# Performance work log

Hardware: AMD Instinct MI355X
Metric: run time of the kernel (lower is better)

The kernel has to match this reference:

```python
import jax, jax.numpy as jnp
import numpy as np

B_, S_, H_, O_ = 4, 2048, 2048, 2048
E_, R_ = 8, 16
LORA_ALPHA = 16.0


def setup_inputs() -> dict:
    key = jax.random.key(0)
    ks = jax.random.split(key, 5)
    x = jax.random.normal(ks[0], (B_, S_, H_), dtype=jnp.float32)
    W = jax.random.normal(ks[1], (O_, H_), dtype=jnp.float32) * 0.02   # frozen base weight [out, in]
    gate_w = jax.random.normal(ks[2], (E_, H_), dtype=jnp.float32) * 0.02  # router Linear weight [E, H]
    A = jax.random.normal(ks[3], (E_, R_, H_), dtype=jnp.float32) * 0.02   # stacked lora_A weights [E, r, in]
    B = jax.random.normal(ks[4], (E_, O_, R_), dtype=jnp.float32) * 0.02   # stacked lora_B weights [E, out, r]
    return {"x": x, "W": W, "gate_w": gate_w, "A": A, "B": B}


def reference(x, W, gate_w, A, B):
    bsz, seq, hid = x.shape
    E = gate_w.shape[0]
    x_flat = x.reshape(-1, hid)                                  # [T, H]

    # base linear
    out = x_flat @ W.T                                           # [T, O]

    # learned router: softmax -> top-2 -> renormalize
    logits = x_flat @ gate_w.T                                   # [T, E]
    probs = jax.nn.softmax(logits, axis=-1)
    topk_w, topk_idx = jax.lax.top_k(probs, 2)                   # [T, 2]
    topk_w = topk_w / jnp.sum(topk_w, axis=-1, keepdims=True)

    # per-token per-expert combine weight (sum over the 2 slots), scaled by alpha
    onehot = jax.nn.one_hot(topk_idx, E, dtype=x.dtype)          # [T, 2, E]
    wmat = jnp.einsum('tk,tke->te', topk_w, onehot) * LORA_ALPHA # [T, E]

    # dense grouped LoRA: h_e = x A_e^T ; out += sum_e w_te * (h_e B_e^T)
    h = jnp.einsum('th,erh->etr', x_flat, A)                     # [E, T, r]
    hw = h * wmat.T[:, :, None]                                  # [E, T, r]
    lora = jnp.einsum('etr,eor->to', hw, B)                      # [T, O]

    return (out + lora).reshape(bsz, seq, -1)
```

## Files before the change

### kernel.cpp

```cpp
#include <hip/hip_runtime.h>
#include <hip/hip_bf16.h>
#include <stdint.h>

#define T_TOK 8192
#define HID   2048
#define OUTD  2048
#define NE    8
#define RR    16
#define KAUG  2176
#define NH    128

typedef __bf16 bf16x8 __attribute__((ext_vector_type(8)));
typedef float  f32x4  __attribute__((ext_vector_type(4)));

#define AS1(p) ((__attribute__((address_space(1))) void*)(p))
#define AS3(p) ((__attribute__((address_space(3))) void*)(p))

__device__ inline unsigned short f2bf(float f) {
  unsigned int u = __builtin_bit_cast(unsigned int, f);
  unsigned int r = (u + 0x7fffu + ((u >> 16) & 1u)) >> 16;
  return (unsigned short)r;
}

__device__ inline ushort4 f2bf4(float4 v) {
  ushort4 u;
  u.x = f2bf(v.x); u.y = f2bf(v.y); u.z = f2bf(v.z); u.w = f2bf(v.w);
  return u;
}

__global__ __launch_bounds__(512) void k_prep(const float* __restrict__ x,
                                              const float* __restrict__ gw,
                                              const float* __restrict__ A,
                                              unsigned short* __restrict__ Xa,
                                              float* __restrict__ wte,
                                              unsigned short* __restrict__ Ag) {
  __shared__ float gws[NE * HID];
  if (blockIdx.x < 1024) {
#pragma unroll
    for (int i = 0; i < 8; ++i) {
      int idx = (i * 512 + (int)threadIdx.x) * 4;
      *(float4*)(gws + idx) = *(const float4*)(gw + idx);
    }
    __syncthreads();
    int w = threadIdx.x >> 6, lane = threadIdx.x & 63;
    int t = blockIdx.x * 8 + w;
    const float* xt = x + (size_t)t * HID;
    unsigned short* xo = Xa + (size_t)t * KAUG;
    double acc[8] = {0, 0, 0, 0, 0, 0, 0, 0};
#pragma unroll
    for (int i = 0; i < 8; ++i) {
      int k = (i * 64 + lane) * 4;
      float4 xv = *(const float4*)(xt + k);
      *(ushort4*)(xo + k) = f2bf4(xv);
#pragma unroll
      for (int e = 0; e < 8; ++e) {
        float4 gv = *(const float4*)(gws + e * HID + k);
        acc[e] += (double)xv.x * gv.x + (double)xv.y * gv.y +
                  (double)xv.z * gv.z + (double)xv.w * gv.w;
      }
    }
#pragma unroll
    for (int off = 32; off >= 1; off >>= 1)
#pragma unroll
      for (int e = 0; e < 8; ++e)
        acc[e] += __shfl_down(acc[e], off, 64);
    if (lane == 0) {
      int e0 = 0; double l0 = acc[0];
#pragma unroll
      for (int e = 1; e < 8; ++e) if (acc[e] > l0) { l0 = acc[e]; e0 = e; }
      int e1 = -1; double l1 = -1e300;
#pragma unroll
      for (int e = 0; e < 8; ++e) if (e != e0 && acc[e] > l1) { l1 = acc[e]; e1 = e; }
      double w0 = 16.0 / (1.0 + exp(l1 - l0));
      float o[8] = {0.f, 0.f, 0.f, 0.f, 0.f, 0.f, 0.f, 0.f};
      o[e0] = (float)w0;
      o[e1] = (float)(16.0 - w0);
      float4* p = (float4*)(wte + (size_t)t * 8);
      p[0] = make_float4(o[0], o[1], o[2], o[3]);
      p[1] = make_float4(o[4], o[5], o[6], o[7]);
    }
  } else {
    int tid = (blockIdx.x - 1024) * 512 + threadIdx.x;
    float4 v = *(const float4*)(A + (size_t)tid * 4);
    *(ushort4*)(Ag + (size_t)tid * 4) = f2bf4(v);
  }
}

__global__ __launch_bounds__(512) void k_ha(const unsigned short* __restrict__ Xa,
                                            const unsigned short* __restrict__ Ag,
                                            const float* __restrict__ wte,
                                            unsigned short* __restrict__ XaW,
                                            const float* __restrict__ W,
                                            const float* __restrict__ Bw,
                                            unsigned short* __restrict__ Wa) {
  __shared__ unsigned short Xs[4][32 * 64];
  __shared__ unsigned short As[4][128 * 64];
  if (blockIdx.x >= 256) {
    int b2 = blockIdx.x - 256;
    if (b2 < 2048) {
      int tid = b2 * 512 + threadIdx.x;
      int row = tid >> 9, c = (tid & 511) << 2;
      float4 v = *(const float4*)(W + (size_t)row * HID + c);
      *(ushort4*)(Wa + (size_t)row * KAUG + c) = f2bf4(v);
    } else {
      int tid = (b2 - 2048) * 512 + threadIdx.x;
      int o = tid >> 5, j = (tid & 31) << 2;
      int e = j >> 4, r = j & 15;
      float4 v = *(const float4*)(Bw + (size_t)e * OUTD * RR + (size_t)o * RR + r);
      *(ushort4*)(Wa + (size_t)o * KAUG + 2048 + j) = f2bf4(v);
    }
    return;
  }

  int tm = blockIdx.x * 32;
  int w = threadIdx.x >> 6, lane = threadIdx.x & 63;
  int wm = (w >> 2) * 16, wn = (w & 3) * 32;
  int lrow = lane >> 3;
  int lcol_s = (lane & 7) << 3;
  int lcol_g = ((lane & 7) ^ (lrow & 7)) << 3;

  const unsigned short* gX = Xa + (size_t)(tm + (w & 3) * 8 + lrow) * KAUG + lcol_g;
  const unsigned short* gA = Ag + (size_t)(w * 16 + lrow) * HID + lcol_g;
  int sxo = ((w & 3) * 8 + lrow) * 64 + lcol_s;
  int sao = (w * 16 + lrow) * 64 + lcol_s;

  f32x4 acc[2] = {};

#define HA_STAGE(slot, koff) do {                                                           \
    if (w < 4)                                                                              \
      __builtin_amdgcn_global_load_lds(AS1(gX + (koff)), AS3(&Xs[slot][0] + sxo), 16, 0, 0);\
    __builtin_amdgcn_global_load_lds(AS1(gA + (koff)), AS3(&As[slot][0] + sao), 16, 0, 0);  \
    __builtin_amdgcn_global_load_lds(AS1(gA + (size_t)8 * HID + (koff)),                    \
                                     AS3(&As[slot][0] + 8 * 64 + sao), 16, 0, 0);           \
  } while (0)

#define HA_COMP(s) do {                                                                     \
    _Pragma("unroll")                                                                       \
    for (int ks = 0; ks < 2; ++ks) {                                                        \
      int kch = ks * 4 + (lane >> 4);                                                       \
      int ko = ((kch ^ (lane & 7)) << 3);                         \
      bf16x8 a = *(const bf16x8*)(&Xs[s][0] + (wm + (lane & 15)) * 64 + ko);                \
      _Pragma("unroll")                                                                     \
      for (int fn = 0; fn < 2; ++fn) {                                                      \
        bf16x8 bv = *(const bf16x8*)(&As[s][0] + (wn + fn * 16 + (lane & 15)) * 64 + ko);   \
        acc[fn] = __builtin_amdgcn_mfma_f32_16x16x32_bf16(a, bv, acc[fn], 0, 0, 0);         \
      }                                                                                     \
    }                                                                                       \
  } while (0)

  HA_STAGE(0, 0);
  HA_STAGE(1, 64);
  HA_STAGE(2, 128);
  for (int t = 0; t < 29; ++t) {
    if (w < 4) asm volatile("s_waitcnt vmcnt(6)" ::: "memory");
    else       asm volatile("s_waitcnt vmcnt(4)" ::: "memory");
    __builtin_amdgcn_s_barrier();
    HA_COMP(t & 3);
    __builtin_amdgcn_s_barrier();
    HA_STAGE((t + 3) & 3, (t + 3) * 64);
  }
  if (w < 4) asm volatile("s_waitcnt vmcnt(6)" ::: "memory");
  else       asm volatile("s_waitcnt vmcnt(4)" ::: "memory");
  __builtin_amdgcn_s_barrier();
  HA_COMP(1);
  if (w < 4) asm volatile("s_waitcnt vmcnt(3)" ::: "memory");
  else       asm volatile("s_waitcnt vmcnt(2)" ::: "memory");
  __builtin_amdgcn_s_barrier();
  HA_COMP(2);
  asm volatile("s_waitcnt vmcnt(0)" ::: "memory");
  __builtin_amdgcn_s_barrier();
  HA_COMP(3);
#undef HA_STAGE
#undef HA_COMP

  int q = lane >> 4;
#pragma unroll
  for (int fn = 0; fn < 2; ++fn) {
    int col = wn + fn * 16 + (lane & 15);
    int e = col >> 4;
#pragma unroll
    for (int r = 0; r < 4; ++r) {
      int t = tm + wm + q * 4 + r;
      float we = wte[(size_t)t * 8 + e];
      XaW[(size_t)t * KAUG + 2048 + col] = f2bf(we * acc[fn][r]);
    }
  }
}

__global__ __launch_bounds__(256, 4) void k_gemm(const unsigned short* __restrict__ Xa,
                                                 const unsigned short* __restrict__ Wa,
                                                 float* __restrict__ out) {
  __shared__ unsigned short As[128 * 64];
  __shared__ unsigned short Bs[128 * 64];
  int lid = blockIdx.x;
  int xcd = lid & 7, s = lid >> 3;
  int bm = (xcd * 8 + (s & 7)) * 128;
  int bn = (s >> 3) * 128;
  int w = threadIdx.x >> 6, lane = threadIdx.x & 63;
  int wm = (w >> 1) * 64, wn = (w & 1) * 64;
  int lrow = lane >> 3;
  int lcol_s = (lane & 7) << 3;
  int lcol_g = ((lane & 7) ^ (lrow & 7)) << 3;

  const unsigned short* gA = Xa + (size_t)(bm + w * 32 + lrow) * KAUG + lcol_g;
  const unsigned short* gB = Wa + (size_t)(bn + w * 32 + lrow) * KAUG + lcol_g;
  unsigned short* sA = As + (w * 32 + lrow) * 64 + lcol_s;
  unsigned short* sB = Bs + (w * 32 + lrow) * 64 + lcol_s;

  f32x4 acc[4][4] = {};
  for (int kt = 0; kt < KAUG; kt += 64) {
#pragma unroll
    for (int i = 0; i < 4; ++i) {
      __builtin_amdgcn_global_load_lds(AS1(gA + (size_t)i * 8 * KAUG), AS3(sA + i * 8 * 64), 16, 0, 0);
      __builtin_amdgcn_global_load_lds(AS1(gB + (size_t)i * 8 * KAUG), AS3(sB + i * 8 * 64), 16, 0, 0);
    }
    __syncthreads();
#pragma unroll
    for (int ks = 0; ks < 2; ++ks) {
      int kch = ks * 4 + (lane >> 4);
      int ko = ((kch ^ (lane & 7)) << 3);
      bf16x8 a[4], b[4];
#pragma unroll
      for (int f = 0; f < 4; ++f) a[f] = *(const bf16x8*)(As + (wm + f * 16 + (lane & 15)) * 64 + ko);
#pragma unroll
      for (int f = 0; f < 4; ++f) b[f] = *(const bf16x8*)(Bs + (wn + f * 16 + (lane & 15)) * 64 + ko);
#pragma unroll
      for (int fm = 0; fm < 4; ++fm)
#pragma unroll
        for (int fn = 0; fn < 4; ++fn)
          acc[fm][fn] = __builtin_amdgcn_mfma_f32_16x16x32_bf16(a[fm], b[fn], acc[fm][fn], 0, 0, 0);
    }
    __syncthreads();
    gA += 64; gB += 64;
  }
#pragma unroll
  for (int fm = 0; fm < 4; ++fm) {
    int row = bm + wm + fm * 16 + ((lane >> 4) << 2);
#pragma unroll
    for (int r = 0; r < 4; ++r) {
      float* orow = out + (size_t)(row + r) * OUTD + bn + wn + (lane & 15);
#pragma unroll
      for (int fn = 0; fn < 4; ++fn) orow[fn * 16] = acc[fm][fn][r];
    }
  }
}

extern "C" void kernel_launch(void* const* d_in, const int* in_sizes, int n_in,
                              void* d_out, int out_size, void* d_ws, size_t ws_size,
                              hipStream_t stream) {
  const float* x  = (const float*)d_in[0];
  const float* W  = (const float*)d_in[1];
  const float* gw = (const float*)d_in[2];
  const float* A  = (const float*)d_in[3];
  const float* B  = (const float*)d_in[4];
  float* out = (float*)d_out;

  char* ws = (char*)d_ws;
  unsigned short* Xa  = (unsigned short*)(ws);
  unsigned short* Wa  = (unsigned short*)(ws + 35651584);
  unsigned short* Ag  = (unsigned short*)(ws + 44564480);
  float*          wte = (float*)        (ws + 45088768);

  k_prep<<<1152, 512, 0, stream>>>(x, gw, A, Xa, wte, Ag);
  k_ha  <<<2432, 512, 0, stream>>>(Xa, Ag, wte, Xa, W, B, Wa);
  k_gemm<<<1024, 256, 0, stream>>>(Xa, Wa, out);
}
```

Baseline: 227.4 us.

## Fuse router/bf16 prep into LoRA-A projection kernel, converting A on the fly

Merges the prep kernel (x to bf16 conversion plus router logits and top-2 weights) into the LoRA-A projection kernel. Each 32-token block now computes its own tokens' routing weights into shared memory, then reads its bf16 x rows back from global. A is loaded as fp32 through registers and converted into LDS in a register-staged 3-slot pipeline, instead of being pre-converted to a separate buffer. This removes one launch and the Ag/wte workspace round trips. The cost is more per-block work, a serial prologue before the MFMA loop, and a dependence on a threadfence making this block's own global Xa writes visible to its later global_load_lds reads.

After: 716.5 us. 3.15x slower.

```diff
diff --git a/kernel.cpp b/kernel.cpp
--- a/kernel.cpp
+++ b/kernel.cpp
@@ -12,6 +12,7 @@
 
 typedef __bf16 bf16x8 __attribute__((ext_vector_type(8)));
 typedef float  f32x4  __attribute__((ext_vector_type(4)));
+typedef unsigned short u16x8 __attribute__((ext_vector_type(8)));
 
 #define AS1(p) ((__attribute__((address_space(1))) void*)(p))
 #define AS3(p) ((__attribute__((address_space(3))) void*)(p))
@@ -28,73 +29,29 @@
   return u;
 }
 
-__global__ __launch_bounds__(512) void k_prep(const float* __restrict__ x,
-                                              const float* __restrict__ gw,
-                                              const float* __restrict__ A,
-                                              unsigned short* __restrict__ Xa,
-                                              float* __restrict__ wte,
-                                              unsigned short* __restrict__ Ag) {
-  __shared__ float gws[NE * HID];
-  if (blockIdx.x < 1024) {
-#pragma unroll
-    for (int i = 0; i < 8; ++i) {
-      int idx = (i * 512 + (int)threadIdx.x) * 4;
-      *(float4*)(gws + idx) = *(const float4*)(gw + idx);
-    }
-    __syncthreads();
-    int w = threadIdx.x >> 6, lane = threadIdx.x & 63;
-    int t = blockIdx.x * 8 + w;
-    const float* xt = x + (size_t)t * HID;
-    unsigned short* xo = Xa + (size_t)t * KAUG;
-    double acc[8] = {0, 0, 0, 0, 0, 0, 0, 0};
-#pragma unroll
-    for (int i = 0; i < 8; ++i) {
-      int k = (i * 64 + lane) * 4;
-      float4 xv = *(const float4*)(xt + k);
-      *(ushort4*)(xo + k) = f2bf4(xv);
-#pragma unroll
-      for (int e = 0; e < 8; ++e) {
-        float4 gv = *(const float4*)(gws + e * HID + k);
-        acc[e] += (double)xv.x * gv.x + (double)xv.y * gv.y +
-                  (double)xv.z * gv.z + (double)xv.w * gv.w;
-      }
-    }
-#pragma unroll
-    for (int off = 32; off >= 1; off >>= 1)
-#pragma unroll
-      for (int e = 0; e < 8; ++e)
-        acc[e] += __shfl_down(acc[e], off, 64);
-    if (lane == 0) {
-      int e0 = 0; double l0 = acc[0];
-#pragma unroll
-      for (int e = 1; e < 8; ++e) if (acc[e] > l0) { l0 = acc[e]; e0 = e; }
-      int e1 = -1; double l1 = -1e300;
-#pragma unroll
-      for (int e = 0; e < 8; ++e) if (e != e0 && acc[e] > l1) { l1 = acc[e]; e1 = e; }
-      double w0 = 16.0 / (1.0 + exp(l1 - l0));
-      float o[8] = {0.f, 0.f, 0.f, 0.f, 0.f, 0.f, 0.f, 0.f};
-      o[e0] = (float)w0;
-      o[e1] = (float)(16.0 - w0);
-      float4* p = (float4*)(wte + (size_t)t * 8);
-      p[0] = make_float4(o[0], o[1], o[2], o[3]);
-      p[1] = make_float4(o[4], o[5], o[6], o[7]);
-    }
-  } else {
-    int tid = (blockIdx.x - 1024) * 512 + threadIdx.x;
-    float4 v = *(const float4*)(A + (size_t)tid * 4);
-    *(ushort4*)(Ag + (size_t)tid * 4) = f2bf4(v);
-  }
-}
-
-__global__ __launch_bounds__(512) void k_ha(const unsigned short* __restrict__ Xa,
-                                            const unsigned short* __restrict__ Ag,
-                                            const float* __restrict__ wte,
-                                            unsigned short* __restrict__ XaW,
-                                            const float* __restrict__ W,
-                                            const float* __restrict__ Bw,
-                                            unsigned short* __restrict__ Wa) {
-  __shared__ unsigned short Xs[4][32 * 64];
-  __shared__ unsigned short As[4][128 * 64];
+__device__ inline void st8(unsigned short* p, float4 a, float4 b) {
+  u16x8 v;
+  v[0] = f2bf(a.x); v[1] = f2bf(a.y); v[2] = f2bf(a.z); v[3] = f2bf(a.w);
+  v[4] = f2bf(b.x); v[5] = f2bf(b.y); v[6] = f2bf(b.z); v[7] = f2bf(b.w);
+  *(u16x8*)p = v;
+}
+
+__global__ __launch_bounds__(512, 4) void k_fused(const float* __restrict__ x,
+                                                  const float* __restrict__ gw,
+                                                  const float* __restrict__ A,
+                                                  const float* __restrict__ W,
+                                                  const float* __restrict__ Bw,
+                                                  unsigned short* __restrict__ Xa,
+                                                  unsigned short* __restrict__ Wa) {
+  __shared__ union {
+    float gws[NE * HID];
+    struct {
+      unsigned short Xs[3][32 * 64];
+      unsigned short As[3][128 * 64];
+    } r;
+  } sh;
+  __shared__ float wte_s[32][8];
+
   if (blockIdx.x >= 256) {
     int b2 = blockIdx.x - 256;
     if (b2 < 2048) {
@@ -112,66 +69,147 @@
     return;
   }
 
+  int w = threadIdx.x >> 6, lane = threadIdx.x & 63;
   int tm = blockIdx.x * 32;
-  int w = threadIdx.x >> 6, lane = threadIdx.x & 63;
+
+#pragma unroll
+  for (int i = 0; i < 8; ++i) {
+    int idx = (i * 512 + (int)threadIdx.x) * 4;
+    *(float4*)(sh.gws + idx) = *(const float4*)(gw + idx);
+  }
+  __syncthreads();
+#pragma unroll 1
+  for (int j = 0; j < 4; ++j) {
+    int t = tm + w * 4 + j;
+    const float* xt = x + (size_t)t * HID;
+    unsigned short* xo = Xa + (size_t)t * KAUG;
+    double acc[8] = {0, 0, 0, 0, 0, 0, 0, 0};
+#pragma unroll
+    for (int i = 0; i < 8; ++i) {
+      int k = (i * 64 + lane) * 4;
+      float4 xv = *(const float4*)(xt + k);
+      *(ushort4*)(xo + k) = f2bf4(xv);
+#pragma unroll
+      for (int e = 0; e < 8; ++e) {
+        float4 gv = *(const float4*)(sh.gws + e * HID + k);
+        acc[e] += (double)xv.x * gv.x + (double)xv.y * gv.y +
+                  (double)xv.z * gv.z + (double)xv.w * gv.w;
+      }
+    }
+#pragma unroll
+    for (int off = 32; off >= 1; off >>= 1)
+#pragma unroll
+      for (int e = 0; e < 8; ++e)
+        acc[e] += __shfl_down(acc[e], off, 64);
+    if (lane == 0) {
+      int e0 = 0; double l0 = acc[0];
+#pragma unroll
+      for (int e = 1; e < 8; ++e) if (acc[e] > l0) { l0 = acc[e]; e0 = e; }
+      int e1 = -1; double l1 = -1e300;
+#pragma unroll
+      for (int e = 0; e < 8; ++e) if (e != e0 && acc[e] > l1) { l1 = acc[e]; e1 = e; }
+      double w0 = 16.0 / (1.0 + exp(l1 - l0));
+      float o[8] = {0.f, 0.f, 0.f, 0.f, 0.f, 0.f, 0.f, 0.f};
+      o[e0] = (float)w0;
+      o[e1] = (float)(16.0 - w0);
+      float4* p = (float4*)(&wte_s[w * 4 + j][0]);
+      p[0] = make_float4(o[0], o[1], o[2], o[3]);
+      p[1] = make_float4(o[4], o[5], o[6], o[7]);
+    }
+  }
+  __threadfence();
+  __syncthreads();
+
+  int wlt4 = (w < 4);
   int wm = (w >> 2) * 16, wn = (w & 3) * 32;
   int lrow = lane >> 3;
   int lcol_s = (lane & 7) << 3;
   int lcol_g = ((lane & 7) ^ (lrow & 7)) << 3;
-
   const unsigned short* gX = Xa + (size_t)(tm + (w & 3) * 8 + lrow) * KAUG + lcol_g;
-  const unsigned short* gA = Ag + (size_t)(w * 16 + lrow) * HID + lcol_g;
   int sxo = ((w & 3) * 8 + lrow) * 64 + lcol_s;
-  int sao = (w * 16 + lrow) * 64 + lcol_s;
-
-  f32x4 acc[2] = {};
-
-#define HA_STAGE(slot, koff) do {                                                           \
-    if (w < 4)                                                                              \
-      __builtin_amdgcn_global_load_lds(AS1(gX + (koff)), AS3(&Xs[slot][0] + sxo), 16, 0, 0);\
-    __builtin_amdgcn_global_load_lds(AS1(gA + (koff)), AS3(&As[slot][0] + sao), 16, 0, 0);  \
-    __builtin_amdgcn_global_load_lds(AS1(gA + (size_t)8 * HID + (koff)),                    \
-                                     AS3(&As[slot][0] + 8 * 64 + sao), 16, 0, 0);           \
-  } while (0)
-
-#define HA_COMP(s) do {                                                                     \
-    _Pragma("unroll")                                                                       \
-    for (int ks = 0; ks < 2; ++ks) {                                                        \
-      int kch = ks * 4 + (lane >> 4);                                                       \
-      int ko = ((kch ^ (lane & 7)) << 3);                         \
-      bf16x8 a = *(const bf16x8*)(&Xs[s][0] + (wm + (lane & 15)) * 64 + ko);                \
-      _Pragma("unroll")                                                                     \
-      for (int fn = 0; fn < 2; ++fn) {                                                      \
-        bf16x8 bv = *(const bf16x8*)(&As[s][0] + (wn + fn * 16 + (lane & 15)) * 64 + ko);   \
-        acc[fn] = __builtin_amdgcn_mfma_f32_16x16x32_bf16(a, bv, acc[fn], 0, 0, 0);         \
-      }                                                                                     \
-    }                                                                                       \
-  } while (0)
-
-  HA_STAGE(0, 0);
-  HA_STAGE(1, 64);
-  HA_STAGE(2, 128);
-  for (int t = 0; t < 29; ++t) {
-    if (w < 4) asm volatile("s_waitcnt vmcnt(6)" ::: "memory");
-    else       asm volatile("s_waitcnt vmcnt(4)" ::: "memory");
-    __builtin_amdgcn_s_barrier();
-    HA_COMP(t & 3);
-    __builtin_amdgcn_s_barrier();
-    HA_STAGE((t + 3) & 3, (t + 3) * 64);
-  }
-  if (w < 4) asm volatile("s_waitcnt vmcnt(6)" ::: "memory");
-  else       asm volatile("s_waitcnt vmcnt(4)" ::: "memory");
+
+  int ia0 = (int)threadIdx.x, ia1 = 512 + (int)threadIdx.x;
+  int colA0 = ia0 >> 3, kgA0 = ia0 & 7;
+  int colA1 = ia1 >> 3, kgA1 = ia1 & 7;
+  const float* gA0 = A + (size_t)colA0 * HID + kgA0 * 8;
+  const float* gA1 = A + (size_t)colA1 * HID + kgA1 * 8;
+  int sa0 = colA0 * 64 + ((kgA0 ^ (colA0 & 7)) << 3);
+  int sa1 = colA1 * 64 + ((kgA1 ^ (colA1 & 7)) << 3);
+
+  f32x4 acc2[2] = {};
+  float4 ab0_0, ab0_1, ab0_2, ab0_3;
+  float4 ab1_0, ab1_1, ab1_2, ab1_3;
+
+#define A_ISSUE(B, T) do {                                            \
+    ab##B##_0 = *(const float4*)(gA0 + (size_t)(T) * 64);             \
+    ab##B##_1 = *(const float4*)(gA0 + (size_t)(T) * 64 + 4);         \
+    ab##B##_2 = *(const float4*)(gA1 + (size_t)(T) * 64);             \
+    ab##B##_3 = *(const float4*)(gA1 + (size_t)(T) * 64 + 4);         \
+  } while (0)
+
+#define CVT_DSW(B, S) do {                                            \
+    st8(&sh.r.As[S][sa0], ab##B##_0, ab##B##_1);                      \
+    st8(&sh.r.As[S][sa1], ab##B##_2, ab##B##_3);                      \
+  } while (0)
+
+#define XS_ISSUE(S, T) do {                                           \
+    if (wlt4)                                                         \
+      __builtin_amdgcn_global_load_lds(AS1(gX + (size_t)(T) * 64),    \
+                                       AS3(&sh.r.Xs[S][0] + sxo), 16, 0, 0); \
+  } while (0)
+
+#define HCOMP(S) do {                                                 \
+    _Pragma("unroll")                                                 \
+    for (int ks = 0; ks < 2; ++ks) {                                  \
+      int kch = ks * 4 + (lane >> 4);                                 \
+      int ko = ((kch ^ (lane & 7)) << 3);                             \
+      bf16x8 av = *(const bf16x8*)(&sh.r.Xs[S][0] + (wm + (lane & 15)) * 64 + ko); \
+      _Pragma("unroll")                                               \
+      for (int fn = 0; fn < 2; ++fn) {                                \
+        bf16x8 bv = *(const bf16x8*)(&sh.r.As[S][0] + (wn + fn * 16 + (lane & 15)) * 64 + ko); \
+        acc2[fn] = __builtin_amdgcn_mfma_f32_16x16x32_bf16(av, bv, acc2[fn], 0, 0, 0); \
+      }                                                               \
+    }                                                                 \
+  } while (0)
+
+#define PH2_BODY(T, ST, SCV, SIS, BCV, BIS) do {                      \
+    if (wlt4) asm volatile("s_waitcnt vmcnt(5) lgkmcnt(0)" ::: "memory"); \
+    else      asm volatile("s_waitcnt lgkmcnt(0)" ::: "memory");      \
+    __builtin_amdgcn_s_barrier();                                     \
+    CVT_DSW(BCV, SCV);                                                \
+    A_ISSUE(BIS, (T) + 2);                                            \
+    XS_ISSUE(SIS, (T) + 2);                                           \
+    HCOMP(ST);                                                        \
+  } while (0)
+
+  A_ISSUE(0, 0);
+  XS_ISSUE(0, 0);
+  A_ISSUE(1, 1);
+  XS_ISSUE(1, 1);
+  CVT_DSW(0, 0);
+
+  for (int tt = 0; tt < 30; tt += 6) {
+    PH2_BODY(tt + 0, 0, 1, 2, 1, 0);
+    PH2_BODY(tt + 1, 1, 2, 0, 0, 1);
+    PH2_BODY(tt + 2, 2, 0, 1, 1, 0);
+    PH2_BODY(tt + 3, 0, 1, 2, 0, 1);
+    PH2_BODY(tt + 4, 1, 2, 0, 1, 0);
+    PH2_BODY(tt + 5, 2, 0, 1, 0, 1);
+  }
+  if (wlt4) asm volatile("s_waitcnt vmcnt(5) lgkmcnt(0)" ::: "memory");
+  else      asm volatile("s_waitcnt lgkmcnt(0)" ::: "memory");
   __builtin_amdgcn_s_barrier();
-  HA_COMP(1);
-  if (w < 4) asm volatile("s_waitcnt vmcnt(3)" ::: "memory");
-  else       asm volatile("s_waitcnt vmcnt(2)" ::: "memory");
+  CVT_DSW(1, 1);
+  HCOMP(0);
+  asm volatile("s_waitcnt vmcnt(0) lgkmcnt(0)" ::: "memory");
   __builtin_amdgcn_s_barrier();
-  HA_COMP(2);
-  asm volatile("s_waitcnt vmcnt(0)" ::: "memory");
-  __builtin_amdgcn_s_barrier();
-  HA_COMP(3);
-#undef HA_STAGE
-#undef HA_COMP
+  HCOMP(1);
+
+#undef A_ISSUE
+#undef CVT_DSW
+#undef XS_ISSUE
+#undef HCOMP
+#undef PH2_BODY
 
   int q = lane >> 4;
 #pragma unroll
@@ -180,9 +218,9 @@
     int e = col >> 4;
 #pragma unroll
     for (int r = 0; r < 4; ++r) {
-      int t = tm + wm + q * 4 + r;
-      float we = wte[(size_t)t * 8 + e];
-      XaW[(size_t)t * KAUG + 2048 + col] = f2bf(we * acc[fn][r]);
+      int tl = wm + q * 4 + r;
+      float we = wte_s[tl][e];
+      Xa[(size_t)(tm + tl) * KAUG + 2048 + col] = f2bf(we * acc2[fn][r]);
     }
   }
 }
@@ -256,12 +294,9 @@
   float* out = (float*)d_out;
 
   char* ws = (char*)d_ws;
-  unsigned short* Xa  = (unsigned short*)(ws);
-  unsigned short* Wa  = (unsigned short*)(ws + 35651584);
-  unsigned short* Ag  = (unsigned short*)(ws + 44564480);
-  float*          wte = (float*)        (ws + 45088768);
-
-  k_prep<<<1152, 512, 0, stream>>>(x, gw, A, Xa, wte, Ag);
-  k_ha  <<<2432, 512, 0, stream>>>(Xa, Ag, wte, Xa, W, B, Wa);
-  k_gemm<<<1024, 256, 0, stream>>>(Xa, Wa, out);
-}
+  unsigned short* Xa = (unsigned short*)(ws);
+  unsigned short* Wa = (unsigned short*)(ws + 35651584);
+
+  k_fused<<<2432, 512, 0, stream>>>(x, gw, A, W, B, Xa, Wa);
+  k_gemm <<<1024, 256, 0, stream>>>(Xa, Wa, out);
+}
```
